# Optimization experiments

Hardware: AMD Instinct MI355X
Metric: run time of the kernel (lower is better)

Reference implementation:

```python
import jax, jax.numpy as jnp
import numpy as np

D_MODEL = 4096
NUM_EXPERTS = 64
TOP_K = 2


def setup_inputs() -> dict:
    key = jax.random.key(0)
    k1, k2 = jax.random.split(key)
    hidden_states = jax.random.normal(k1, (4, 4096, D_MODEL), dtype=jnp.float32)
    # nn.Linear(d_model, num_experts, bias=False) weight: [num_experts, d_model]
    W = jax.random.normal(k2, (NUM_EXPERTS, D_MODEL), dtype=jnp.float32) * (1.0 / np.sqrt(D_MODEL))
    return {"hidden_states": hidden_states, "W": W}


def reference(hidden_states, W):
    # router_logits: [B, S, E]
    router_logits = jnp.einsum("bsd,ed->bse", hidden_states, W)
    # top-k over experts (torch.topk returns values sorted descending; lax.top_k matches)
    top_k_logits, top_k_indices = jax.lax.top_k(router_logits, TOP_K)
    routing_weights = jax.nn.softmax(top_k_logits, axis=-1)
    return routing_weights, top_k_indices
```

## Files before the change

kernel.cpp:

```cpp
#include <hip/hip_runtime.h>
#include <stdint.h>

#define D_MODEL  4096
#define N_EXP    64
#define N_TOK    16384
#define MTILE    16
#define KSTEP    32
#define KQ       1024
#define NSTEP    (KQ / KSTEP)

typedef float  f32x4  __attribute__((ext_vector_type(4)));
typedef short  bf16x8 __attribute__((ext_vector_type(8)));

__device__ __forceinline__ void cvt8(float4 v0, float4 v1, bf16x8& hi, bf16x8& lo) {
  float f[8] = {v0.x, v0.y, v0.z, v0.w, v1.x, v1.y, v1.z, v1.w};
#pragma unroll
  for (int i = 0; i < 8; ++i) {
    unsigned u  = __builtin_bit_cast(unsigned, f[i]);
    unsigned r  = u + 0x7FFFu + ((u >> 16) & 1u);
    unsigned hb = r & 0xFFFF0000u;
    float    res = f[i] - __builtin_bit_cast(float, hb);
    hi[i] = (short)(hb >> 16);
    lo[i] = (short)(__builtin_bit_cast(unsigned, res) >> 16);
  }
}

__global__ __launch_bounds__(256) void SimpleMoERouter_54219667144993_kernel(
    const float* __restrict__ X, const float* __restrict__ W,
    float* __restrict__ outw, float* __restrict__ outi)
{
  __shared__ float sRed[4][MTILE][N_EXP + 4];

  const int tid  = threadIdx.x;
  const int lane = tid & 63;
  const int wv   = tid >> 6;
  const int tok0 = blockIdx.x * MTILE;
  const int r16  = lane & 15;
  const int kq   = lane >> 4;

  const float* xp = X + (size_t)(tok0 + r16) * D_MODEL + wv * KQ + kq * 8;
  const float* wp = W + (size_t)r16 * D_MODEL + wv * KQ + kq * 8;

  f32x4 acc[4] = {{0.f,0.f,0.f,0.f},{0.f,0.f,0.f,0.f},
                  {0.f,0.f,0.f,0.f},{0.f,0.f,0.f,0.f}};

  float4 xa = *(const float4*)xp;
  float4 xb = *(const float4*)(xp + 4);

  for (int s = 0; s < NSTEP; ++s) {
    const int off = s * KSTEP;
    float4 nxa, nxb;
    if (s + 1 < NSTEP) {
      nxa = *(const float4*)(xp + off + KSTEP);
      nxb = *(const float4*)(xp + off + KSTEP + 4);
    }
    bf16x8 ah, al;
    cvt8(xa, xb, ah, al);
#pragma unroll
    for (int nt = 0; nt < 4; ++nt) {
      const float* wq = wp + (size_t)(nt * 16) * D_MODEL + off;
      float4 wa = *(const float4*)wq;
      float4 wb = *(const float4*)(wq + 4);
      bf16x8 bh, bl;
      cvt8(wa, wb, bh, bl);
      acc[nt] = __builtin_amdgcn_mfma_f32_16x16x32_bf16(ah, bh, acc[nt], 0, 0, 0);
      acc[nt] = __builtin_amdgcn_mfma_f32_16x16x32_bf16(ah, bl, acc[nt], 0, 0, 0);
      acc[nt] = __builtin_amdgcn_mfma_f32_16x16x32_bf16(al, bh, acc[nt], 0, 0, 0);
    }
    xa = nxa; xb = nxb;
  }

#pragma unroll
  for (int nt = 0; nt < 4; ++nt) {
#pragma unroll
    for (int r = 0; r < 4; ++r) {
      sRed[wv][kq * 4 + r][nt * 16 + r16] = acc[nt][r];
    }
  }
  __syncthreads();

  if (tid < MTILE) {
    float best = -3.4e38f, sec = -3.4e38f;
    int bi = 0, si = 0;
#pragma unroll 8
    for (int e = 0; e < N_EXP; ++e) {
      const float v = sRed[0][tid][e] + sRed[1][tid][e]
                    + sRed[2][tid][e] + sRed[3][tid][e];
      const bool b1 = v > best;
      const bool b2 = v > sec;
      sec  = b1 ? best : (b2 ? v : sec);
      si   = b1 ? bi   : (b2 ? e : si);
      best = b1 ? v : best;
      bi   = b1 ? e : bi;
    }
    const float ed  = expf(sec - best);
    const float inv = 1.0f / (1.0f + ed);
    const int gt = tok0 + tid;
    outw[2 * gt]     = inv;
    outw[2 * gt + 1] = ed * inv;
    outi[2 * gt]     = (float)bi;
    outi[2 * gt + 1] = (float)si;
  }
}

extern "C" void kernel_launch(void* const* d_in, const int* in_sizes, int n_in,
                              void* d_out, int out_size, void* d_ws, size_t ws_size,
                              hipStream_t stream) {
  const float* X = (const float*)d_in[0];
  const float* W = (const float*)d_in[1];
  float* outw = (float*)d_out;
  float* outi = (float*)d_out + (size_t)N_TOK * 2;
  hipLaunchKernelGGL(SimpleMoERouter_54219667144993_kernel,
                     dim3(N_TOK / MTILE), dim3(256), 0, stream,
                     X, W, outw, outi);
}
```

Measured before the change: 428.9 us.

## Pre-split W into bf16 hi/lo and stage X tiles via async LDS loads

```diff
diff --git a/kernel.cpp b/kernel.cpp
--- a/kernel.cpp
+++ b/kernel.cpp
@@ -1,13 +1,12 @@
 #include <hip/hip_runtime.h>
 #include <stdint.h>
 
-#define D_MODEL  4096
-#define N_EXP    64
-#define N_TOK    16384
-#define MTILE    16
-#define KSTEP    32
-#define KQ       1024
-#define NSTEP    (KQ / KSTEP)
+#define D_MODEL 4096
+#define N_EXP   64
+#define N_TOK   16384
+#define MTILE   32
+#define KC      128
+#define NCHUNK  (D_MODEL / KC)
 
 typedef float  f32x4  __attribute__((ext_vector_type(4)));
 typedef short  bf16x8 __attribute__((ext_vector_type(8)));
@@ -25,11 +24,27 @@
   }
 }
 
+__global__ __launch_bounds__(256) void prep_w_kernel(
+    const float* __restrict__ W, short* __restrict__ Wh, short* __restrict__ Wl)
+{
+  const int t  = blockIdx.x * 256 + threadIdx.x;
+  const int e  = t & 63;
+  const int kg = t >> 6;
+  const float* src = W + (size_t)e * D_MODEL + kg * 8;
+  float4 a = *(const float4*)src;
+  float4 b = *(const float4*)(src + 4);
+  bf16x8 hi, lo;
+  cvt8(a, b, hi, lo);
+  *(bf16x8*)(Wh + ((size_t)kg * 64 + e) * 8) = hi;
+  *(bf16x8*)(Wl + ((size_t)kg * 64 + e) * 8) = lo;
+}
+
 __global__ __launch_bounds__(256) void SimpleMoERouter_54219667144993_kernel(
-    const float* __restrict__ X, const float* __restrict__ W,
-    float* __restrict__ outw, float* __restrict__ outi)
+    const float* __restrict__ X, const short* __restrict__ Wh,
+    const short* __restrict__ Wl, float* __restrict__ outw, float* __restrict__ outi)
 {
-  __shared__ float sRed[4][MTILE][N_EXP + 4];
+  __shared__ uint4 sX[2][MTILE * KC / 4];
+  __shared__ float sRed[MTILE][N_EXP + 1];
 
   const int tid  = threadIdx.x;
   const int lane = tid & 63;
@@ -37,46 +52,63 @@
   const int tok0 = blockIdx.x * MTILE;
   const int r16  = lane & 15;
   const int kq   = lane >> 4;
+  const int mh   = wv & 1;
+  const int nh   = wv >> 1;
+  const int arow = mh * 16 + r16;
+  const int rs   = arow & 15;
 
-  const float* xp = X + (size_t)(tok0 + r16) * D_MODEL + wv * KQ + kq * 8;
-  const float* wp = W + (size_t)r16 * D_MODEL + wv * KQ + kq * 8;
+  const float* xbase = X + (size_t)tok0 * D_MODEL;
 
-  f32x4 acc[4] = {{0.f,0.f,0.f,0.f},{0.f,0.f,0.f,0.f},
-                  {0.f,0.f,0.f,0.f},{0.f,0.f,0.f,0.f}};
+  auto STAGE = [&](int c, int b) {
+#pragma unroll
+    for (int q = 0; q < 4; ++q) {
+      const int G   = q * 256 + tid;
+      const int row = G >> 5;
+      const int col = G & 31;
+      const int sc  = col ^ (row & 15);
+      const float* src = xbase + (size_t)row * D_MODEL + (size_t)c * KC + sc * 4;
+      __builtin_amdgcn_global_load_lds(
+          (const __attribute__((address_space(1))) void*)src,
+          (__attribute__((address_space(3))) void*)&sX[b][q * 256 + wv * 64],
+          16, 0, 0);
+    }
+  };
 
-  float4 xa = *(const float4*)xp;
-  float4 xb = *(const float4*)(xp + 4);
+  f32x4 acc[2] = {{0.f,0.f,0.f,0.f},{0.f,0.f,0.f,0.f}};
 
-  for (int s = 0; s < NSTEP; ++s) {
-    const int off = s * KSTEP;
-    float4 nxa, nxb;
-    if (s + 1 < NSTEP) {
-      nxa = *(const float4*)(xp + off + KSTEP);
-      nxb = *(const float4*)(xp + off + KSTEP + 4);
+  STAGE(0, 0);
+  __syncthreads();
+
+  int b = 0;
+  for (int c = 0; c < NCHUNK; ++c) {
+    if (c + 1 < NCHUNK) STAGE(c + 1, b ^ 1);
+#pragma unroll
+    for (int s = 0; s < 4; ++s) {
+      const int cg = s * 8 + kq * 2;
+      uint4 g0 = sX[b][arow * 32 + (cg ^ rs)];
+      uint4 g1 = sX[b][arow * 32 + ((cg + 1) ^ rs)];
+      bf16x8 ah, al;
+      cvt8(__builtin_bit_cast(float4, g0), __builtin_bit_cast(float4, g1), ah, al);
+      const size_t wg = ((size_t)c * 16 + s * 4 + kq) * 64;
+#pragma unroll
+      for (int j = 0; j < 2; ++j) {
+        const size_t wi = (wg + (size_t)(nh * 2 + j) * 16 + r16) * 8;
+        bf16x8 bh = *(const bf16x8*)(Wh + wi);
+        bf16x8 bl = *(const bf16x8*)(Wl + wi);
+        acc[j] = __builtin_amdgcn_mfma_f32_16x16x32_bf16(ah, bh, acc[j], 0, 0, 0);
+        acc[j] = __builtin_amdgcn_mfma_f32_16x16x32_bf16(ah, bl, acc[j], 0, 0, 0);
+        acc[j] = __builtin_amdgcn_mfma_f32_16x16x32_bf16(al, bh, acc[j], 0, 0, 0);
+      }
     }
-    bf16x8 ah, al;
-    cvt8(xa, xb, ah, al);
-#pragma unroll
-    for (int nt = 0; nt < 4; ++nt) {
-      const float* wq = wp + (size_t)(nt * 16) * D_MODEL + off;
-      float4 wa = *(const float4*)wq;
-      float4 wb = *(const float4*)(wq + 4);
-      bf16x8 bh, bl;
-      cvt8(wa, wb, bh, bl);
-      acc[nt] = __builtin_amdgcn_mfma_f32_16x16x32_bf16(ah, bh, acc[nt], 0, 0, 0);
-      acc[nt] = __builtin_amdgcn_mfma_f32_16x16x32_bf16(ah, bl, acc[nt], 0, 0, 0);
-      acc[nt] = __builtin_amdgcn_mfma_f32_16x16x32_bf16(al, bh, acc[nt], 0, 0, 0);
-    }
-    xa = nxa; xb = nxb;
+    __syncthreads();
+    b ^= 1;
   }
 
 #pragma unroll
-  for (int nt = 0; nt < 4; ++nt) {
+  for (int j = 0; j < 2; ++j)
 #pragma unroll
-    for (int r = 0; r < 4; ++r) {
-      sRed[wv][kq * 4 + r][nt * 16 + r16] = acc[nt][r];
-    }
-  }
+    for (int r = 0; r < 4; ++r)
+      sRed[mh * 16 + kq * 4 + r][nh * 32 + j * 16 + r16] = acc[j][r];
   __syncthreads();
 
   if (tid < MTILE) {
@@ -84,8 +116,7 @@
     int bi = 0, si = 0;
 #pragma unroll 8
     for (int e = 0; e < N_EXP; ++e) {
-      const float v = sRed[0][tid][e] + sRed[1][tid][e]
-                    + sRed[2][tid][e] + sRed[3][tid][e];
+      const float v = sRed[tid][e];
       const bool b1 = v > best;
       const bool b2 = v > sec;
       sec  = b1 ? best : (b2 ? v : sec);
@@ -110,7 +141,11 @@
   const float* W = (const float*)d_in[1];
   float* outw = (float*)d_out;
   float* outi = (float*)d_out + (size_t)N_TOK * 2;
+  short* Wh = (short*)d_ws;
+  short* Wl = (short*)d_ws + (size_t)N_EXP * D_MODEL;
+
+  hipLaunchKernelGGL(prep_w_kernel, dim3(128), dim3(256), 0, stream, W, Wh, Wl);
   hipLaunchKernelGGL(SimpleMoERouter_54219667144993_kernel,
                      dim3(N_TOK / MTILE), dim3(256), 0, stream,
-                     X, W, outw, outi);
+                     X, Wh, Wl, outw, outi);
 }
```

New measurement: 420.4 us. 1.02x faster.
